# Kernel optimization log

Hardware: AMD Instinct MI355X
Metric: run time of the kernel (lower is better)

## Reference

```python
import jax, jax.numpy as jnp
import numpy as np
from jax import lax

B, T, V, E, H, M = 512, 60, 50000, 300, 512, 256


def _lstm_final_h(x_emb, seqlen, kernel, bias):
    """BasicLSTMCell (gate order i,j,f,o; forget_bias=1.0) with dynamic_rnn
    sequence_length semantics: state stops updating at t >= seqlen.
    x_emb: [B, T, E]; returns final h: [B, H]."""
    b = x_emb.shape[0]
    h0 = jnp.zeros((b, H), x_emb.dtype)
    c0 = jnp.zeros((b, H), x_emb.dtype)

    def step(carry, inp):
        c, h = carry
        xt, t = inp
        z = jnp.concatenate([xt, h], axis=1) @ kernel + bias  # [B, 4H]
        i, j, f, o = jnp.split(z, 4, axis=1)
        nc = c * jax.nn.sigmoid(f + 1.0) + jax.nn.sigmoid(i) * jnp.tanh(j)
        nh = jnp.tanh(nc) * jax.nn.sigmoid(o)
        valid = (t < seqlen)[:, None]
        return (jnp.where(valid, nc, c), jnp.where(valid, nh, h)), None

    (c, h), _ = lax.scan(step, (c0, h0),
                         (jnp.swapaxes(x_emb, 0, 1), jnp.arange(T)))
    return h


def setup_inputs() -> dict:
    key = jax.random.key(0)
    ks = jax.random.split(key, 8)
    return {
        "input1": jax.random.randint(ks[0], (B, T), 0, V, dtype=jnp.int32),
        "input2": jax.random.randint(ks[1], (B, T), 0, V, dtype=jnp.int32),
        "seqlen1": jax.random.randint(ks[2], (B,), 1, T + 1, dtype=jnp.int32),
        "seqlen2": jax.random.randint(ks[3], (B,), 1, T + 1, dtype=jnp.int32),
        "embeddings": jax.random.normal(ks[4], (V, E), jnp.float32) * 0.1,
        "lstm_kernel": jax.random.normal(ks[5], (E + H, 4 * H), jnp.float32) * 0.02,
        "lstm_bias": jnp.zeros((4 * H,), jnp.float32),
        "W1": jax.random.normal(ks[6], (4 * (H + 1) + 1, M), jnp.float32) * 0.02,
        "b1": jnp.zeros((1, M), jnp.float32),
        "W2": jax.random.normal(ks[7], (M, 2), jnp.float32) * 0.02,
        "b2": jnp.zeros((1, 2), jnp.float32),
    }


def reference(input1, input2, seqlen1, seqlen2, embeddings,
              lstm_kernel, lstm_bias, W1, b1, W2, b2):
    x1 = embeddings[input1]  # [B, T, E]
    x2 = embeddings[input2]
    h1 = _lstm_final_h(x1, seqlen1, lstm_kernel, lstm_bias)  # [B, H]
    h2 = _lstm_final_h(x2, seqlen2, lstm_kernel, lstm_bias)
    len1 = (seqlen1.astype(jnp.float32) / float(T))[:, None]
    len2 = (seqlen2.astype(jnp.float32) / float(T))[:, None]
    h1 = jnp.concatenate([h1, len1], axis=1)  # [B, H+1]
    h2 = jnp.concatenate([h2, len2], axis=1)
    h_sub = h1 - h2
    h_dist = jnp.sum(h_sub * h_sub, axis=1, keepdims=True)  # [B, 1]
    h_mul = h1 * h2
    h_combined = jnp.concatenate([h1, h2, h_sub, h_dist, h_mul], axis=1)
    e1 = jax.nn.relu(h_combined @ W1 + b1)  # dropout keep_prob=1 -> identity
    preds = e1 @ W2 + b2  # [B, 2]
    return preds
```

## Files before the change

### kernel.cpp

```cpp
#include <hip/hip_runtime.h>
#include <hip/hip_bf16.h>

#define BATCH 512
#define TT 60
#define EDIM 300
#define HDIM 512
#define KREAL 812
#define KP 896
#define KP1 2112
#define MDIM 256

typedef __bf16 bf16x4 __attribute__((ext_vector_type(4)));
typedef __bf16 bf16x8 __attribute__((ext_vector_type(8)));
typedef float  f32x16 __attribute__((ext_vector_type(16)));

#define GLL16(g, l) __builtin_amdgcn_global_load_lds( \
    (const __attribute__((address_space(1))) void*)(g), \
    (__attribute__((address_space(3))) void*)(l), 16, 0, 0)

__device__ __forceinline__ float sigm(float x) {
    return 1.0f / (1.0f + __expf(-x));
}
__device__ __forceinline__ float tanh_fast(float x) {
    float e = __expf(-2.0f * fabsf(x));
    float r = (1.0f - e) / (1.0f + e);
    return x >= 0.0f ? r : -r;
}


__global__ __launch_bounds__(256) void sort_rows(const int* __restrict__ sl1,
                                                 const int* __restrict__ sl2,
                                                 int* __restrict__ rowinfo,
                                                 unsigned* __restrict__ nact) {
    __shared__ unsigned cnt[61];
    __shared__ unsigned off[61];
    int tid = threadIdx.x;
    if (tid < 61) cnt[tid] = 0;
    __syncthreads();
    for (int i = tid; i < 1024; i += 256) {
        int sl = (i < 512) ? sl1[i] : sl2[i - 512];
        atomicAdd(&cnt[60 - sl], 1u);
    }
    __syncthreads();
    if (tid == 0) {
        unsigned s = 0;
        for (int k = 0; k < 61; ++k) { off[k] = s; s += cnt[k]; }
        for (int t = 0; t < 60; ++t) {
            unsigned act = off[60 - t];
            nact[t] = (act + 63) >> 6;
        }
    }
    __syncthreads();
    for (int i = tid; i < 1024; i += 256) {
        int sc = i >= 512;
        int b = i & 511;
        int sl = sc ? sl2[b] : sl1[b];
        unsigned pos = atomicAdd(&off[60 - sl], 1u);
        rowinfo[pos] = b | (sc << 15) | (sl << 20);
    }
}

__global__ __launch_bounds__(256) void prep_w(const float* __restrict__ kern,
                                              __bf16* __restrict__ wf) {
    __shared__ float tile[64][65];
    int bk = blockIdx.x % 14;
    int bn = blockIdx.x / 14;
    int k0 = bk * 64, n0 = bn * 64;
    int tid = threadIdx.x;
#pragma unroll
    for (int i = 0; i < 16; ++i) {
        int id = i * 256 + tid;
        int kk = id >> 6, nn = id & 63;
        int kg = k0 + kk;
        int src = (kg < 300) ? kg : (kg >= 384 ? kg - 84 : -1);
        tile[kk][nn] = (src >= 0) ? kern[(size_t)src * 2048 + n0 + nn] : 0.0f;
    }
    __syncthreads();
    int gate = n0 >> 9;
    int nt = gate >> 1;
#pragma unroll
    for (int i = 0; i < 2; ++i) {
        int id = i * 256 + tid;
        int nn = id >> 3, k8 = id & 7;
        bf16x8 hv, lv;
#pragma unroll
        for (int j = 0; j < 8; ++j) {
            float v = tile[k8 * 8 + j][nn];
            __bf16 h = (__bf16)v;
            hv[j] = h;
            lv[j] = (__bf16)(v - (float)h);
        }
        int cg = (((n0 & 511) >> 4) + (nn >> 4));
        int hc = nn & 15;
        int lzc = ((gate & 1) << 4) + hc;
        int kglob = k0 + k8 * 8;
        int c = kglob >> 7;
        int j = (kglob >> 4) & 7;
        int half = k8 & 1;
        size_t o = (size_t)cg * 114688 + c * 16384 + (j * 4 + nt * 2) * 512
                 + (half * 32 + lzc) * 8;
        *(bf16x8*)(wf + o) = hv;
        *(bf16x8*)(wf + o + 512) = lv;
    }
}

__global__ __launch_bounds__(256) void prep_w1(const float* __restrict__ W1,
                                               __bf16* __restrict__ w1h,
                                               __bf16* __restrict__ w1l) {
    __shared__ float tile[64][65];
    int bk = blockIdx.x % 33;
    int bn = blockIdx.x / 33;
    int k0 = bk * 64, n0 = bn * 64;
    int tid = threadIdx.x;
#pragma unroll
    for (int i = 0; i < 16; ++i) {
        int id = i * 256 + tid;
        int kk = id >> 6, nn = id & 63;
        int kg = k0 + kk;
        tile[kk][nn] = (kg < 2053) ? W1[(size_t)kg * MDIM + n0 + nn] : 0.0f;
    }
    __syncthreads();
#pragma unroll
    for (int i = 0; i < 2; ++i) {
        int id = i * 256 + tid;
        int nn = id >> 3, k8 = (id & 7) * 8;
        bf16x8 hv, lv;
#pragma unroll
        for (int j = 0; j < 8; ++j) {
            float v = tile[k8 + j][nn];
            __bf16 h = (__bf16)v;
            hv[j] = h;
            lv[j] = (__bf16)(v - (float)h);
        }
        size_t o = (size_t)(n0 + nn) * KP1 + k0 + k8;
        *(bf16x8*)(w1h + o) = hv;
        *(bf16x8*)(w1l + o) = lv;
    }
}

__device__ __forceinline__ void emb_unit(int tok, int rl, int rr, int bt,
                                         const float* __restrict__ emb,
                                         __bf16* Xfn) {
    const float* er = emb + (size_t)tok * EDIM + rr * 8;
    float4 f0 = *(const float4*)er;
    float4 f1 = (rr == 37) ? make_float4(0.f, 0.f, 0.f, 0.f)
                           : *(const float4*)(er + 4);
    float vv[8] = {f0.x, f0.y, f0.z, f0.w, f1.x, f1.y, f1.z, f1.w};
    bf16x8 hv, lv;
#pragma unroll
    for (int j = 0; j < 8; ++j) {
        __bf16 h = (__bf16)vv[j];
        hv[j] = h;
        lv[j] = (__bf16)(vv[j] - (float)h);
    }
    int ke = rr * 8;
    int c = ke >> 7, kl = ke & 127;
    int kg = kl >> 6, jj = (kl >> 4) & 3, half = (kl >> 3) & 1;
    int s = rl >> 5;
    size_t base = ((((size_t)bt * 2 + s) * 2 + kg) * 7 + c) * 4096 + jj * 1024
                + (half * 32 + (rl & 31)) * 8;
    *(bf16x8*)(Xfn + base) = hv;
    *(bf16x8*)(Xfn + base + 512) = lv;
}

__global__ __launch_bounds__(256) void prep_x0(const int* __restrict__ in1,
                                               const int* __restrict__ in2,
                                               const int* __restrict__ rowinfo,
                                               const float* __restrict__ emb,
                                               __bf16* __restrict__ Xf) {
    __shared__ int tk[64];
    int bt = blockIdx.x >> 5, cg = blockIdx.x & 31;
    int tid = threadIdx.x;
    if (tid < 64) {
        int info = rowinfo[bt * 64 + tid];
        int b = info & 511, sc = (info >> 15) & 1;
        tk[tid] = (sc ? in2 : in1)[b * TT];
    }
    __syncthreads();
    if (tid < 76) {
        int id = tid * 32 + cg;
        int rl = id / 38, rr = id - rl * 38;
        emb_unit(tk[rl], rl, rr, bt, emb, Xf);
    }
}

#define ZSTR 72

__global__ __launch_bounds__(256, 2) void lstm_step(
    int t,
    const int* __restrict__ in1, const int* __restrict__ in2,
    const int* __restrict__ rowinfo, const unsigned* __restrict__ nact,
    const float* __restrict__ emb, const float* __restrict__ bias,
    const __bf16* __restrict__ wf,
    const __bf16* __restrict__ Xf, __bf16* __restrict__ Xfn,
    float* __restrict__ h_state, float* __restrict__ c_state) {

    int bx = blockIdx.x;
    int xcd = bx & 7;
    int loc = bx >> 3;
    int bt = ((loc >> 3) << 1) | (xcd & 1);
    int cg = ((xcd >> 1) << 3) | (loc & 7);
    if (bt >= (int)nact[t]) return;

    __shared__ __align__(16) __bf16 Bb[2][16384];
    __shared__ int info_s[64];
    __shared__ int tk[64];

    int tid = threadIdx.x;
    int w = tid >> 6, lane = tid & 63, l31 = lane & 31;
    int s = w >> 1, kg = w & 1;

    if (tid < 64) {
        int info = rowinfo[bt * 64 + tid];
        info_s[tid] = info;
        int b = info & 511, sc = (info >> 15) & 1;
        int tn = (t + 1 < TT) ? t + 1 : t;
        tk[tid] = (sc ? in2 : in1)[b * TT + tn];
    }

    const __bf16* wb = wf + (size_t)cg * 114688;
    auto stageB = [&](int c, int buf) {
        const __bf16* src = wb + c * 16384 + w * 4096 + lane * 8;
        __bf16* dst = &Bb[buf][w * 4096 + lane * 8];
#pragma unroll
        for (int i = 0; i < 8; ++i)
            GLL16(src + i * 512, dst + i * 512);
    };

    const __bf16* Abase = Xf + ((((size_t)bt * 2 + s) * 2 + kg) * 7) * 4096
                        + lane * 8;

    f32x16 acc[2];
#pragma unroll
    for (int nt = 0; nt < 2; ++nt)
#pragma unroll
        for (int r = 0; r < 16; ++r) acc[nt][r] = 0.0f;

    bf16x8 aH[4], aL[4];
    stageB(0, 0);
#pragma unroll
    for (int jj = 0; jj < 4; ++jj) {
        aH[jj] = *(const bf16x8*)(Abase + jj * 1024);
        aL[jj] = *(const bf16x8*)(Abase + jj * 1024 + 512);
    }
    __syncthreads();

#pragma unroll
    for (int c = 0; c < 7; ++c) {
        int cur = c & 1;
        bf16x8 nH[4], nL[4];
        if (c < 6) {
            stageB(c + 1, 1 - cur);
            const __bf16* An = Abase + (c + 1) * 4096;
#pragma unroll
            for (int jj = 0; jj < 4; ++jj) {
                nH[jj] = *(const bf16x8*)(An + jj * 1024);
                nL[jj] = *(const bf16x8*)(An + jj * 1024 + 512);
            }
        }
#pragma unroll
        for (int jj = 0; jj < 4; ++jj) {
            int j = kg * 4 + jj;
#pragma unroll
            for (int nt = 0; nt < 2; ++nt) {
                int T0 = (j * 4 + nt * 2) * 512 + lane * 8;
                bf16x8 bh = *(const bf16x8*)(&Bb[cur][T0]);
                bf16x8 bl = *(const bf16x8*)(&Bb[cur][T0 + 512]);
                acc[nt] = __builtin_amdgcn_mfma_f32_32x32x16_bf16(aH[jj], bh, acc[nt], 0, 0, 0);
                acc[nt] = __builtin_amdgcn_mfma_f32_32x32x16_bf16(aH[jj], bl, acc[nt], 0, 0, 0);
                acc[nt] = __builtin_amdgcn_mfma_f32_32x32x16_bf16(aL[jj], bh, acc[nt], 0, 0, 0);
            }
        }
        if (c < 6) {
#pragma unroll
            for (int jj = 0; jj < 4; ++jj) { aH[jj] = nH[jj]; aL[jj] = nL[jj]; }
        }
        __syncthreads();
    }

    float* zs = (float*)&Bb[1][0];
    if (kg == 0) {
#pragma unroll
        for (int nt = 0; nt < 2; ++nt)
#pragma unroll
            for (int r = 0; r < 16; ++r) {
                int rl = s * 32 + (r & 3) + ((r >> 2) << 3) + ((lane >> 5) << 2);
                zs[rl * ZSTR + nt * 32 + l31] = acc[nt][r];
            }
    }
    __syncthreads();
    if (kg == 1) {
#pragma unroll
        for (int nt = 0; nt < 2; ++nt)
#pragma unroll
            for (int r = 0; r < 16; ++r) {
                int rl = s * 32 + (r & 3) + ((r >> 2) << 3) + ((lane >> 5) << 2);
                zs[rl * ZSTR + nt * 32 + l31] += acc[nt][r];
            }
    }
    __syncthreads();

    __bf16* zh = &Bb[0][0];
    int hc16 = tid & 15;
    int hcol = (cg << 4) + hc16;
    float bi = bias[hcol], bj = bias[512 + hcol];
    float bfv = bias[1024 + hcol], bo = bias[1536 + hcol];
#pragma unroll
    for (int i = 0; i < 4; ++i) {
        int rl = i * 16 + (tid >> 4);
        int info = info_s[rl];
        int b = info & 511, sc = (info >> 15) & 1, sl = info >> 20;
        float zi = zs[rl * ZSTR + hc16]      + bi;
        float zj = zs[rl * ZSTR + 16 + hc16] + bj;
        float zf = zs[rl * ZSTR + 32 + hc16] + bfv;
        float zo = zs[rl * ZSTR + 48 + hc16] + bo;
        size_t co = (size_t)(bt * 64 + rl) * HDIM + hcol;
        size_t ho = (size_t)((sc << 9) + b) * HDIM + hcol;
        float c_old = c_state[co];
        float h_old = h_state[ho];
        float nc = c_old * sigm(zf + 1.0f) + sigm(zi) * tanh_fast(zj);
        float nh = tanh_fast(nc) * sigm(zo);
        bool valid = t < sl;
        float cs = valid ? nc : c_old;
        float hs = valid ? nh : h_old;
        c_state[co] = cs;
        h_state[ho] = hs;
        __bf16 hh = (__bf16)hs;
        int grp = hc16 >> 3, e = hc16 & 7;
        zh[(grp * 64 + rl) * 8 + e] = hh;
        zh[((2 + grp) * 64 + rl) * 8 + e] = (__bf16)(hs - (float)hh);
    }
    __syncthreads();

    if (t + 1 < TT) {
        int plane = tid >> 7;
        int grp = (tid >> 6) & 1;
        int rl = tid & 63;
        bf16x8 val = *(const bf16x8*)(zh + ((plane * 2 + grp) * 64 + rl) * 8);
        int s2 = rl >> 5;
        int c2 = 3 + (cg >> 3);
        int kg2 = (cg >> 2) & 1;
        int jj2 = cg & 3;
        size_t base = ((((size_t)bt * 2 + s2) * 2 + kg2) * 7 + c2) * 4096
                    + jj2 * 1024 + plane * 512 + (grp * 32 + (rl & 31)) * 8;
        *(bf16x8*)(Xfn + base) = val;
        if (tid < 76) {
            int id = tid * 32 + cg;
            int rl2 = id / 38, rr = id - rl2 * 38;
            emb_unit(tk[rl2], rl2, rr, bt, emb, Xfn);
        }
    }
}

__global__ __launch_bounds__(256) void head1(const float* __restrict__ h_state,
                                             const int* __restrict__ sl1,
                                             const int* __restrict__ sl2,
                                             __bf16* __restrict__ hch,
                                             __bf16* __restrict__ hcl) {
    int b = blockIdx.x;
    int tid = threadIdx.x;
    const float* h1 = h_state + (size_t)b * HDIM;
    const float* h2 = h_state + (size_t)(512 + b) * HDIM;
    size_t ro = (size_t)b * KP1;
    float l1 = (float)sl1[b] / (float)TT;
    float l2 = (float)sl2[b] / (float)TT;
    float part = 0.0f;
#pragma unroll
    for (int i = 0; i < 2; ++i) {
        int k = i * 256 + tid;
        float a = h1[k], c = h2[k];
        float sv = a - c;
        float mv = a * c;
        __bf16 xh;
        xh = (__bf16)a;  hch[ro + k] = xh;         hcl[ro + k] = (__bf16)(a - (float)xh);
        xh = (__bf16)c;  hch[ro + 513 + k] = xh;   hcl[ro + 513 + k] = (__bf16)(c - (float)xh);
        xh = (__bf16)sv; hch[ro + 1026 + k] = xh;  hcl[ro + 1026 + k] = (__bf16)(sv - (float)xh);
        xh = (__bf16)mv; hch[ro + 1540 + k] = xh;  hcl[ro + 1540 + k] = (__bf16)(mv - (float)xh);
        part += sv * sv;
    }
    __shared__ float red[4];
#pragma unroll
    for (int off = 32; off > 0; off >>= 1) part += __shfl_down(part, off, 64);
    if ((tid & 63) == 0) red[tid >> 6] = part;
    __syncthreads();
    if (tid == 0) {
        float d = red[0] + red[1] + red[2] + red[3];
        float ls = l1 - l2;
        d += ls * ls;
        float vals[5] = {l1, l2, ls, d, l1 * l2};
        int pos[5] = {512, 1025, 1538, 1539, 2052};
#pragma unroll
        for (int i = 0; i < 5; ++i) {
            __bf16 xh = (__bf16)vals[i];
            hch[ro + pos[i]] = xh;
            hcl[ro + pos[i]] = (__bf16)(vals[i] - (float)xh);
        }
    }
}

__global__ __launch_bounds__(512, 2) void head2m(
    const __bf16* __restrict__ hch, const __bf16* __restrict__ hcl,
    const __bf16* __restrict__ w1h, const __bf16* __restrict__ w1l,
    float* __restrict__ part) {

    __shared__ __align__(16) __bf16 Bb[2][64 * 512];

    int tid = threadIdx.x;
    int bx = blockIdx.x;
    int mt = bx >> 3;
    int n2 = (bx >> 2) & 1;
    int ks = bx & 3;
    int w = tid >> 6, lane = tid & 63, l31 = lane & 31;
    int half8 = (lane >> 5) << 3;
    int s = w >> 1, nh = w & 1;
    int kbase = ks * 528;

    int k8 = tid & 15;
    int jb = k8 >> 1;
    int rb = (tid >> 4) & 31;
    size_t gboff[8];
    int lo[8];
#pragma unroll
    for (int i = 0; i < 8; ++i) {
        int r = ((i & 3) << 5) + rb;
        int plane = i >> 2;
        int ng = n2 * 128 + r;
        gboff[i] = (size_t)ng * KP1 + k8 * 8;
        int nt = r >> 5;
        int colp = ((r & 31) + (jb << 2)) & 31;
        lo[i] = ((((jb << 2) + nt) << 1) + plane) * 512 + (colp + ((k8 & 1) << 5)) * 8;
    }

    const __bf16* Ah0 = hch + (size_t)(mt * 128 + s * 32 + l31) * KP1 + kbase + half8;
    const __bf16* Al0 = hcl + (size_t)(mt * 128 + s * 32 + l31) * KP1 + kbase + half8;

    bf16x8 rB[8];
    f32x16 acc[2];
#pragma unroll
    for (int nt = 0; nt < 2; ++nt)
#pragma unroll
        for (int r = 0; r < 16; ++r) acc[nt][r] = 0.0f;

#pragma unroll
    for (int i = 0; i < 8; ++i)
        rB[i] = *(const bf16x8*)(((i >= 4) ? w1l : w1h) + gboff[i] + kbase);
#pragma unroll
    for (int i = 0; i < 8; ++i) *(bf16x8*)(&Bb[0][lo[i]]) = rB[i];
    __syncthreads();

    for (int c = 0; c < 5; ++c) {
        int cur = c & 1;
        if (c < 4) {
            int k0 = kbase + (c + 1) * 128;
            bool tail = (c + 1 == 4);
#pragma unroll
            for (int i = 0; i < 8; ++i) {
                if (!tail || k8 < 2)
                    rB[i] = *(const bf16x8*)(((i >= 4) ? w1l : w1h) + gboff[i] + k0);
            }
        }
        int jmax = (c == 4) ? 1 : 8;
        for (int j = 0; j < jmax; ++j) {
            bf16x8 ah = *(const bf16x8*)(Ah0 + c * 128 + j * 16);
            bf16x8 al = *(const bf16x8*)(Al0 + c * 128 + j * 16);
            int cp = ((l31 + (j << 2)) & 31) + ((lane >> 5) << 5);
#pragma unroll
            for (int ntl = 0; ntl < 2; ++ntl) {
                int ntg = nh * 2 + ntl;
                const __bf16* bp = &Bb[cur][(((j << 2) + ntg) << 1) * 512 + cp * 8];
                bf16x8 bh = *(const bf16x8*)bp;
                bf16x8 bl = *(const bf16x8*)(bp + 512);
                acc[ntl] = __builtin_amdgcn_mfma_f32_32x32x16_bf16(ah, bh, acc[ntl], 0, 0, 0);
                acc[ntl] = __builtin_amdgcn_mfma_f32_32x32x16_bf16(ah, bl, acc[ntl], 0, 0, 0);
                acc[ntl] = __builtin_amdgcn_mfma_f32_32x32x16_bf16(al, bh, acc[ntl], 0, 0, 0);
            }
        }
        if (c < 4) {
#pragma unroll
            for (int i = 0; i < 8; ++i) *(bf16x8*)(&Bb[1 - cur][lo[i]]) = rB[i];
        }
        __syncthreads();
    }

#pragma unroll
    for (int ntl = 0; ntl < 2; ++ntl)
#pragma unroll
        for (int r = 0; r < 16; ++r) {
            int row = mt * 128 + s * 32 + (r & 3) + ((r >> 2) << 3) + ((lane >> 5) << 2);
            int col = n2 * 128 + nh * 64 + ntl * 32 + l31;
            part[((size_t)ks * 512 + row) * MDIM + col] = acc[ntl][r];
        }
}

__global__ __launch_bounds__(256) void head3(const float* __restrict__ part,
                                             const float* __restrict__ b1,
                                             const float* __restrict__ W2,
                                             const float* __restrict__ b2,
                                             float* __restrict__ out) {
    int row = blockIdx.x;
    int tid = threadIdx.x;
    float sv = b1[tid];
#pragma unroll
    for (int ks = 0; ks < 4; ++ks)
        sv += part[((size_t)ks * 512 + row) * MDIM + tid];
    float e = fmaxf(sv, 0.0f);
    float p0 = e * W2[tid * 2 + 0];
    float p1 = e * W2[tid * 2 + 1];
#pragma unroll
    for (int off = 32; off > 0; off >>= 1) {
        p0 += __shfl_down(p0, off, 64);
        p1 += __shfl_down(p1, off, 64);
    }
    __shared__ float r0[4], r1[4];
    if ((tid & 63) == 0) { r0[tid >> 6] = p0; r1[tid >> 6] = p1; }
    __syncthreads();
    if (tid == 0) out[row * 2 + 0] = r0[0] + r0[1] + r0[2] + r0[3] + b2[0];
    if (tid == 1) out[row * 2 + 1] = r1[0] + r1[1] + r1[2] + r1[3] + b2[1];
}

extern "C" void kernel_launch(void* const* d_in, const int* in_sizes, int n_in,
                              void* d_out, int out_size, void* d_ws, size_t ws_size,
                              hipStream_t stream) {
    const int*   in1  = (const int*)d_in[0];
    const int*   in2  = (const int*)d_in[1];
    const int*   sl1  = (const int*)d_in[2];
    const int*   sl2  = (const int*)d_in[3];
    const float* emb  = (const float*)d_in[4];
    const float* kern = (const float*)d_in[5];
    const float* bias = (const float*)d_in[6];
    const float* W1   = (const float*)d_in[7];
    const float* b1   = (const float*)d_in[8];
    const float* W2   = (const float*)d_in[9];
    const float* b2   = (const float*)d_in[10];
    float* out = (float*)d_out;

    char* ws = (char*)d_ws;
    int*      rowinfo = (int*)ws;
    unsigned* nact    = (unsigned*)(ws + 4096u);
    float*  h_state = (float*)(ws + 2097152u);
    float*  c_state = (float*)(ws + 4194304u);
    __bf16* Xf0 = (__bf16*)(ws + 6291456u);
    __bf16* Xf1 = (__bf16*)(ws + 9961472u);
    __bf16* wf  = (__bf16*)(ws + 13631488u);
    __bf16* hch = (__bf16*)(ws + 20971520u);
    __bf16* hcl = (__bf16*)(ws + 23134208u);
    __bf16* w1h = (__bf16*)(ws + 25296896u);
    __bf16* w1l = (__bf16*)(ws + 26378240u);
    float*  part = (float*)(ws + 27459584u);

    hipMemsetAsync(ws + 2097152u, 0, 7864320u, stream);
    hipMemsetAsync(ws + 20971520u, 0, 4325376u, stream);

    sort_rows<<<dim3(1), dim3(256), 0, stream>>>(sl1, sl2, rowinfo, nact);
    prep_w<<<dim3(14 * 32), dim3(256), 0, stream>>>(kern, wf);
    prep_w1<<<dim3(33 * 4), dim3(256), 0, stream>>>(W1, w1h, w1l);
    prep_x0<<<dim3(512), dim3(256), 0, stream>>>(in1, in2, rowinfo, emb, Xf0);

    for (int t = 0; t < TT; ++t) {
        __bf16* Xf  = (t & 1) ? Xf1 : Xf0;
        __bf16* Xfn = (t & 1) ? Xf0 : Xf1;
        lstm_step<<<dim3(512), dim3(256), 0, stream>>>(
            t, in1, in2, rowinfo, nact, emb, bias, wf, Xf, Xfn,
            h_state, c_state);
    }

    head1<<<dim3(512), dim3(256), 0, stream>>>(h_state, sl1, sl2, hch, hcl);
    head2m<<<dim3(32), dim3(512), 0, stream>>>(hch, hcl, w1h, w1l, part);
    head3<<<dim3(512), dim3(256), 0, stream>>>(part, b1, W2, b2, out);
}
```

Before: 1.066 ms.

## Replace per-timestep LSTM launches with one persistent kernel using per-tile flags

The 60 per-timestep kernel launches become a single persistent kernel. Each row tile loops over its own timesteps and waits on an atomic step counter until all 32 column-group blocks have written the previous hidden state into a per-timestep buffer. The whole embedding table is pre-converted once into split bf16 hi/lo form, so the step loop reads embedding rows directly instead of re-gathering and scattering them. This removes launch overhead and lets tiles with short sequences finish early. In exchange it depends on all 512 blocks being co-resident (two per CU), adds spin-wait latency, and converting the full 50000-row table costs extra bandwidth.

```diff
diff --git a/kernel.cpp b/kernel.cpp
--- a/kernel.cpp
+++ b/kernel.cpp
@@ -5,10 +5,9 @@
 #define TT 60
 #define EDIM 300
 #define HDIM 512
-#define KREAL 812
-#define KP 896
 #define KP1 2112
 #define MDIM 256
+#define V48 2400000
 
 typedef __bf16 bf16x4 __attribute__((ext_vector_type(4)));
 typedef __bf16 bf16x8 __attribute__((ext_vector_type(8)));
@@ -31,11 +30,12 @@
 __global__ __launch_bounds__(256) void sort_rows(const int* __restrict__ sl1,
                                                  const int* __restrict__ sl2,
                                                  int* __restrict__ rowinfo,
-                                                 unsigned* __restrict__ nact) {
+                                                 unsigned* __restrict__ step_done) {
     __shared__ unsigned cnt[61];
     __shared__ unsigned off[61];
     int tid = threadIdx.x;
     if (tid < 61) cnt[tid] = 0;
+    if (tid >= 64 && tid < 80) step_done[tid - 64] = 0;
     __syncthreads();
     for (int i = tid; i < 1024; i += 256) {
         int sl = (i < 512) ? sl1[i] : sl2[i - 512];
@@ -45,10 +45,6 @@
     if (tid == 0) {
         unsigned s = 0;
         for (int k = 0; k < 61; ++k) { off[k] = s; s += cnt[k]; }
-        for (int t = 0; t < 60; ++t) {
-            unsigned act = off[60 - t];
-            nact[t] = (act + 63) >> 6;
-        }
     }
     __syncthreads();
     for (int i = tid; i < 1024; i += 256) {
@@ -138,14 +134,28 @@
     }
 }
 
-__device__ __forceinline__ void emb_unit(int tok, int rl, int rr, int bt,
-                                         const float* __restrict__ emb,
-                                         __bf16* Xfn) {
-    const float* er = emb + (size_t)tok * EDIM + rr * 8;
-    float4 f0 = *(const float4*)er;
-    float4 f1 = (rr == 37) ? make_float4(0.f, 0.f, 0.f, 0.f)
-                           : *(const float4*)(er + 4);
-    float vv[8] = {f0.x, f0.y, f0.z, f0.w, f1.x, f1.y, f1.z, f1.w};
+__global__ __launch_bounds__(256) void prep_emb(const float* __restrict__ emb,
+                                                __bf16* __restrict__ embB) {
+    int id = blockIdx.x * 256 + threadIdx.x;
+    if (id >= V48) return;
+    int tok = id / 48;
+    int k8 = id - tok * 48;
+    int k0 = k8 * 8;
+    float vv[8];
+    const float* er = emb + (size_t)tok * EDIM + k0;
+    if (k0 + 8 <= EDIM) {
+        float4 f0 = *(const float4*)er;
+        float4 f1 = *(const float4*)(er + 4);
+        vv[0] = f0.x; vv[1] = f0.y; vv[2] = f0.z; vv[3] = f0.w;
+        vv[4] = f1.x; vv[5] = f1.y; vv[6] = f1.z; vv[7] = f1.w;
+    } else if (k0 < EDIM) {
+        float4 f0 = *(const float4*)er;
+        vv[0] = f0.x; vv[1] = f0.y; vv[2] = f0.z; vv[3] = f0.w;
+        vv[4] = vv[5] = vv[6] = vv[7] = 0.f;
+    } else {
+#pragma unroll
+        for (int j = 0; j < 8; ++j) vv[j] = 0.f;
+    }
     bf16x8 hv, lv;
 #pragma unroll
     for (int j = 0; j < 8; ++j) {
@@ -153,46 +163,20 @@
         hv[j] = h;
         lv[j] = (__bf16)(vv[j] - (float)h);
     }
-    int ke = rr * 8;
-    int c = ke >> 7, kl = ke & 127;
-    int kg = kl >> 6, jj = (kl >> 4) & 3, half = (kl >> 3) & 1;
-    int s = rl >> 5;
-    size_t base = ((((size_t)bt * 2 + s) * 2 + kg) * 7 + c) * 4096 + jj * 1024
-                + (half * 32 + (rl & 31)) * 8;
-    *(bf16x8*)(Xfn + base) = hv;
-    *(bf16x8*)(Xfn + base + 512) = lv;
-}
-
-__global__ __launch_bounds__(256) void prep_x0(const int* __restrict__ in1,
-                                               const int* __restrict__ in2,
-                                               const int* __restrict__ rowinfo,
-                                               const float* __restrict__ emb,
-                                               __bf16* __restrict__ Xf) {
-    __shared__ int tk[64];
-    int bt = blockIdx.x >> 5, cg = blockIdx.x & 31;
-    int tid = threadIdx.x;
-    if (tid < 64) {
-        int info = rowinfo[bt * 64 + tid];
-        int b = info & 511, sc = (info >> 15) & 1;
-        tk[tid] = (sc ? in2 : in1)[b * TT];
-    }
-    __syncthreads();
-    if (tid < 76) {
-        int id = tid * 32 + cg;
-        int rl = id / 38, rr = id - rl * 38;
-        emb_unit(tk[rl], rl, rr, bt, emb, Xf);
-    }
+    size_t o = (size_t)tok * 768 + k0;
+    *(bf16x8*)(embB + o) = hv;
+    *(bf16x8*)(embB + o + 384) = lv;
 }
 
 #define ZSTR 72
 
-__global__ __launch_bounds__(256, 2) void lstm_step(
-    int t,
+__global__ __launch_bounds__(256, 2) void lstm_all(
     const int* __restrict__ in1, const int* __restrict__ in2,
-    const int* __restrict__ rowinfo, const unsigned* __restrict__ nact,
-    const float* __restrict__ emb, const float* __restrict__ bias,
+    const int* __restrict__ rowinfo,
+    const __bf16* __restrict__ embB, const float* __restrict__ bias,
     const __bf16* __restrict__ wf,
-    const __bf16* __restrict__ Xf, __bf16* __restrict__ Xfn,
+    __bf16* __restrict__ XfH,
+    unsigned* __restrict__ step_done,
     float* __restrict__ h_state, float* __restrict__ c_state) {
 
     int bx = blockIdx.x;
@@ -200,23 +184,26 @@
     int loc = bx >> 3;
     int bt = ((loc >> 3) << 1) | (xcd & 1);
     int cg = ((xcd >> 1) << 3) | (loc & 7);
-    if (bt >= (int)nact[t]) return;
 
     __shared__ __align__(16) __bf16 Bb[2][16384];
     __shared__ int info_s[64];
-    __shared__ int tk[64];
 
     int tid = threadIdx.x;
     int w = tid >> 6, lane = tid & 63, l31 = lane & 31;
     int s = w >> 1, kg = w & 1;
 
-    if (tid < 64) {
-        int info = rowinfo[bt * 64 + tid];
-        info_s[tid] = info;
-        int b = info & 511, sc = (info >> 15) & 1;
-        int tn = (t + 1 < TT) ? t + 1 : t;
-        tk[tid] = (sc ? in2 : in1)[b * TT + tn];
-    }
+    if (tid < 64) info_s[tid] = rowinfo[bt * 64 + tid];
+    __syncthreads();
+    int t_end = info_s[0] >> 20;
+
+    int rowl = s * 32 + l31;
+    int inf_r = info_s[rowl];
+    const int* tokptr = ((((inf_r >> 15) & 1) ? in2 : in1)) + (inf_r & 511) * TT;
+
+    int hc16 = tid & 15;
+    int hcol = (cg << 4) + hc16;
+    float bi = bias[hcol], bj = bias[512 + hcol];
+    float bfv = bias[1024 + hcol], bo = bias[1536 + hcol];
 
     const __bf16* wb = wf + (size_t)cg * 114688;
     auto stageB = [&](int c, int buf) {
@@ -227,128 +214,148 @@
             GLL16(src + i * 512, dst + i * 512);
     };
 
-    const __bf16* Abase = Xf + ((((size_t)bt * 2 + s) * 2 + kg) * 7) * 4096
-                        + lane * 8;
-
-    f32x16 acc[2];
-#pragma unroll
-    for (int nt = 0; nt < 2; ++nt)
-#pragma unroll
-        for (int r = 0; r < 16; ++r) acc[nt][r] = 0.0f;
-
-    bf16x8 aH[4], aL[4];
-    stageB(0, 0);
-#pragma unroll
-    for (int jj = 0; jj < 4; ++jj) {
-        aH[jj] = *(const bf16x8*)(Abase + jj * 1024);
-        aL[jj] = *(const bf16x8*)(Abase + jj * 1024 + 512);
-    }
-    __syncthreads();
-
-#pragma unroll
-    for (int c = 0; c < 7; ++c) {
-        int cur = c & 1;
-        bf16x8 nH[4], nL[4];
-        if (c < 6) {
-            stageB(c + 1, 1 - cur);
-            const __bf16* An = Abase + (c + 1) * 4096;
+    int ew = kg * 64 + ((lane >> 5) << 3);
+    size_t hw_off = (size_t)((s * 2 + kg) * 4) * 4096 + lane * 8;
+
+    for (int t = 0; t < t_end; ++t) {
+        f32x16 acc[2];
+#pragma unroll
+        for (int nt = 0; nt < 2; ++nt)
+#pragma unroll
+            for (int r = 0; r < 16; ++r) acc[nt][r] = 0.0f;
+
+        int tok = tokptr[t];
+        const __bf16* eb = embB + (size_t)tok * 768 + ew;
+        const __bf16* hrd = XfH + ((size_t)t * 16 + bt) * 65536 + hw_off;
+
+        bf16x8 aH[4], aL[4];
+        stageB(0, 0);
+#pragma unroll
+        for (int jj = 0; jj < 4; ++jj) {
+            aH[jj] = *(const bf16x8*)(eb + jj * 16);
+            aL[jj] = *(const bf16x8*)(eb + 384 + jj * 16);
+        }
+
+        if (t > 0 && tid == 0) {
+            unsigned target = 32u * (unsigned)t;
+            int guard = 0;
+            while (__hip_atomic_load(step_done + bt, __ATOMIC_RELAXED,
+                                     __HIP_MEMORY_SCOPE_AGENT) < target) {
+                __builtin_amdgcn_s_sleep(4);
+                if (++guard > (1 << 20)) break;
+            }
+        }
+        __syncthreads();
+
+#pragma unroll
+        for (int c = 0; c < 7; ++c) {
+            int cur = c & 1;
+            bf16x8 nH[4], nL[4];
+            if (c < 6) {
+                stageB(c + 1, 1 - cur);
+                if (c < 2) {
+                    const __bf16* en = eb + (c + 1) * 128;
+#pragma unroll
+                    for (int jj = 0; jj < 4; ++jj) {
+                        nH[jj] = *(const bf16x8*)(en + jj * 16);
+                        nL[jj] = *(const bf16x8*)(en + 384 + jj * 16);
+                    }
+                } else {
+                    const __bf16* An = hrd + (c - 2) * 4096;
+#pragma unroll
+                    for (int jj = 0; jj < 4; ++jj) {
+                        nH[jj] = *(const bf16x8*)(An + jj * 1024);
+                        nL[jj] = *(const bf16x8*)(An + jj * 1024 + 512);
+                    }
+                }
+            }
 #pragma unroll
             for (int jj = 0; jj < 4; ++jj) {
-                nH[jj] = *(const bf16x8*)(An + jj * 1024);
-                nL[jj] = *(const bf16x8*)(An + jj * 1024 + 512);
+                int j = kg * 4 + jj;
+#pragma unroll
+                for (int nt = 0; nt < 2; ++nt) {
+                    int T0 = (j * 4 + nt * 2) * 512 + lane * 8;
+                    bf16x8 bh = *(const bf16x8*)(&Bb[cur][T0]);
+                    bf16x8 bl = *(const bf16x8*)(&Bb[cur][T0 + 512]);
+                    acc[nt] = __builtin_amdgcn_mfma_f32_32x32x16_bf16(aH[jj], bh, acc[nt], 0, 0, 0);
+                    acc[nt] = __builtin_amdgcn_mfma_f32_32x32x16_bf16(aH[jj], bl, acc[nt], 0, 0, 0);
+                    acc[nt] = __builtin_amdgcn_mfma_f32_32x32x16_bf16(aL[jj], bh, acc[nt], 0, 0, 0);
+                }
             }
-        }
-#pragma unroll
-        for (int jj = 0; jj < 4; ++jj) {
-            int j = kg * 4 + jj;
-#pragma unroll
-            for (int nt = 0; nt < 2; ++nt) {
-                int T0 = (j * 4 + nt * 2) * 512 + lane * 8;
-                bf16x8 bh = *(const bf16x8*)(&Bb[cur][T0]);
-                bf16x8 bl = *(const bf16x8*)(&Bb[cur][T0 + 512]);
-                acc[nt] = __builtin_amdgcn_mfma_f32_32x32x16_bf16(aH[jj], bh, acc[nt], 0, 0, 0);
-                acc[nt] = __builtin_amdgcn_mfma_f32_32x32x16_bf16(aH[jj], bl, acc[nt], 0, 0, 0);
-                acc[nt] = __builtin_amdgcn_mfma_f32_32x32x16_bf16(aL[jj], bh, acc[nt], 0, 0, 0);
+            if (c < 6) {
+#pragma unroll
+                for (int jj = 0; jj < 4; ++jj) { aH[jj] = nH[jj]; aL[jj] = nL[jj]; }
             }
-        }
-        if (c < 6) {
-#pragma unroll
-            for (int jj = 0; jj < 4; ++jj) { aH[jj] = nH[jj]; aL[jj] = nL[jj]; }
+            __syncthreads();
+        }
+
+        float* zs = (float*)&Bb[1][0];
+        if (kg == 0) {
+#pragma unroll
+            for (int nt = 0; nt < 2; ++nt)
+#pragma unroll
+                for (int r = 0; r < 16; ++r) {
+                    int rl = s * 32 + (r & 3) + ((r >> 2) << 3) + ((lane >> 5) << 2);
+                    zs[rl * ZSTR + nt * 32 + l31] = acc[nt][r];
+                }
         }
         __syncthreads();
-    }
-
-    float* zs = (float*)&Bb[1][0];
-    if (kg == 0) {
-#pragma unroll
-        for (int nt = 0; nt < 2; ++nt)
-#pragma unroll
-            for (int r = 0; r < 16; ++r) {
-                int rl = s * 32 + (r & 3) + ((r >> 2) << 3) + ((lane >> 5) << 2);
-                zs[rl * ZSTR + nt * 32 + l31] = acc[nt][r];
-            }
-    }
-    __syncthreads();
-    if (kg == 1) {
-#pragma unroll
-        for (int nt = 0; nt < 2; ++nt)
-#pragma unroll
-            for (int r = 0; r < 16; ++r) {
-                int rl = s * 32 + (r & 3) + ((r >> 2) << 3) + ((lane >> 5) << 2);
-                zs[rl * ZSTR + nt * 32 + l31] += acc[nt][r];
-            }
-    }
-    __syncthreads();
-
-    __bf16* zh = &Bb[0][0];
-    int hc16 = tid & 15;
-    int hcol = (cg << 4) + hc16;
-    float bi = bias[hcol], bj = bias[512 + hcol];
-    float bfv = bias[1024 + hcol], bo = bias[1536 + hcol];
-#pragma unroll
-    for (int i = 0; i < 4; ++i) {
-        int rl = i * 16 + (tid >> 4);
-        int info = info_s[rl];
-        int b = info & 511, sc = (info >> 15) & 1, sl = info >> 20;
-        float zi = zs[rl * ZSTR + hc16]      + bi;
-        float zj = zs[rl * ZSTR + 16 + hc16] + bj;
-        float zf = zs[rl * ZSTR + 32 + hc16] + bfv;
-        float zo = zs[rl * ZSTR + 48 + hc16] + bo;
-        size_t co = (size_t)(bt * 64 + rl) * HDIM + hcol;
-        size_t ho = (size_t)((sc << 9) + b) * HDIM + hcol;
-        float c_old = c_state[co];
-        float h_old = h_state[ho];
-        float nc = c_old * sigm(zf + 1.0f) + sigm(zi) * tanh_fast(zj);
-        float nh = tanh_fast(nc) * sigm(zo);
-        bool valid = t < sl;
-        float cs = valid ? nc : c_old;
-        float hs = valid ? nh : h_old;
-        c_state[co] = cs;
-        h_state[ho] = hs;
-        __bf16 hh = (__bf16)hs;
-        int grp = hc16 >> 3, e = hc16 & 7;
-        zh[(grp * 64 + rl) * 8 + e] = hh;
-        zh[((2 + grp) * 64 + rl) * 8 + e] = (__bf16)(hs - (float)hh);
-    }
-    __syncthreads();
-
-    if (t + 1 < TT) {
-        int plane = tid >> 7;
-        int grp = (tid >> 6) & 1;
-        int rl = tid & 63;
-        bf16x8 val = *(const bf16x8*)(zh + ((plane * 2 + grp) * 64 + rl) * 8);
-        int s2 = rl >> 5;
-        int c2 = 3 + (cg >> 3);
-        int kg2 = (cg >> 2) & 1;
-        int jj2 = cg & 3;
-        size_t base = ((((size_t)bt * 2 + s2) * 2 + kg2) * 7 + c2) * 4096
-                    + jj2 * 1024 + plane * 512 + (grp * 32 + (rl & 31)) * 8;
-        *(bf16x8*)(Xfn + base) = val;
-        if (tid < 76) {
-            int id = tid * 32 + cg;
-            int rl2 = id / 38, rr = id - rl2 * 38;
-            emb_unit(tk[rl2], rl2, rr, bt, emb, Xfn);
-        }
+        if (kg == 1) {
+#pragma unroll
+            for (int nt = 0; nt < 2; ++nt)
+#pragma unroll
+                for (int r = 0; r < 16; ++r) {
+                    int rl = s * 32 + (r & 3) + ((r >> 2) << 3) + ((lane >> 5) << 2);
+                    zs[rl * ZSTR + nt * 32 + l31] += acc[nt][r];
+                }
+        }
+        __syncthreads();
+
+        __bf16* zh = &Bb[0][0];
+#pragma unroll
+        for (int i = 0; i < 4; ++i) {
+            int rl = i * 16 + (tid >> 4);
+            int info = info_s[rl];
+            int b = info & 511, sc = (info >> 15) & 1, sl = info >> 20;
+            float zi = zs[rl * ZSTR + hc16]      + bi;
+            float zj = zs[rl * ZSTR + 16 + hc16] + bj;
+            float zf = zs[rl * ZSTR + 32 + hc16] + bfv;
+            float zo = zs[rl * ZSTR + 48 + hc16] + bo;
+            size_t co = (size_t)(bt * 64 + rl) * HDIM + hcol;
+            size_t ho = (size_t)((sc << 9) + b) * HDIM + hcol;
+            float c_old = c_state[co];
+            float h_old = h_state[ho];
+            float nc = c_old * sigm(zf + 1.0f) + sigm(zi) * tanh_fast(zj);
+            float nh = tanh_fast(nc) * sigm(zo);
+            bool valid = t < sl;
+            float cs = valid ? nc : c_old;
+            float hs = valid ? nh : h_old;
+            c_state[co] = cs;
+            h_state[ho] = hs;
+            __bf16 hh = (__bf16)hs;
+            int grp = hc16 >> 3, e = hc16 & 7;
+            zh[(grp * 64 + rl) * 8 + e] = hh;
+            zh[((2 + grp) * 64 + rl) * 8 + e] = (__bf16)(hs - (float)hh);
+        }
+        __syncthreads();
+
+        if (t + 1 < t_end) {
+            int plane = tid >> 7;
+            int grp = (tid >> 6) & 1;
+            int rl = tid & 63;
+            ulonglong2 uv = *(const ulonglong2*)(zh + ((plane * 2 + grp) * 64 + rl) * 8);
+            int s2 = rl >> 5;
+            size_t base = ((size_t)(t + 1) * 16 + bt) * 65536
+                        + (size_t)((s2 * 2 + ((cg >> 2) & 1)) * 4 + (cg >> 3)) * 4096
+                        + (cg & 3) * 1024 + plane * 512 + (grp * 32 + (rl & 31)) * 8;
+            unsigned long long* dst = (unsigned long long*)(XfH + base);
+            __hip_atomic_store(dst,     uv.x, __ATOMIC_RELAXED, __HIP_MEMORY_SCOPE_AGENT);
+            __hip_atomic_store(dst + 1, uv.y, __ATOMIC_RELAXED, __HIP_MEMORY_SCOPE_AGENT);
+        }
+        __syncthreads();
+        if (t + 1 < t_end && tid == 0)
+            __hip_atomic_fetch_add(step_done + bt, 1u, __ATOMIC_RELEASE,
+                                   __HIP_MEMORY_SCOPE_AGENT);
     }
 }
 
@@ -535,34 +542,30 @@
     float* out = (float*)d_out;
 
     char* ws = (char*)d_ws;
-    int*      rowinfo = (int*)ws;
-    unsigned* nact    = (unsigned*)(ws + 4096u);
+    int*      rowinfo   = (int*)ws;
+    unsigned* step_done = (unsigned*)(ws + 4096u);
     float*  h_state = (float*)(ws + 2097152u);
     float*  c_state = (float*)(ws + 4194304u);
-    __bf16* Xf0 = (__bf16*)(ws + 6291456u);
-    __bf16* Xf1 = (__bf16*)(ws + 9961472u);
-    __bf16* wf  = (__bf16*)(ws + 13631488u);
-    __bf16* hch = (__bf16*)(ws + 20971520u);
-    __bf16* hcl = (__bf16*)(ws + 23134208u);
-    __bf16* w1h = (__bf16*)(ws + 25296896u);
-    __bf16* w1l = (__bf16*)(ws + 26378240u);
-    float*  part = (float*)(ws + 27459584u);
-
-    hipMemsetAsync(ws + 2097152u, 0, 7864320u, stream);
-    hipMemsetAsync(ws + 20971520u, 0, 4325376u, stream);
-
-    sort_rows<<<dim3(1), dim3(256), 0, stream>>>(sl1, sl2, rowinfo, nact);
+    __bf16* wf   = (__bf16*)(ws + 6291456u);
+    __bf16* hch  = (__bf16*)(ws + 13631488u);
+    __bf16* hcl  = (__bf16*)(ws + 15794176u);
+    __bf16* w1h  = (__bf16*)(ws + 17956864u);
+    __bf16* w1l  = (__bf16*)(ws + 19038208u);
+    float*  part = (float*)(ws + 20119552u);
+    __bf16* embB = (__bf16*)(ws + 23068672u);
+    __bf16* XfH  = (__bf16*)(ws + 100663296u);
+
+    hipMemsetAsync(ws + 2097152u, 0, 4194304u, stream);
+    hipMemsetAsync(ws + 13631488u, 0, 4325376u, stream);
+    hipMemsetAsync(ws + 100663296u, 0, 2097152u, stream);
+
+    sort_rows<<<dim3(1), dim3(256), 0, stream>>>(sl1, sl2, rowinfo, step_done);
     prep_w<<<dim3(14 * 32), dim3(256), 0, stream>>>(kern, wf);
     prep_w1<<<dim3(33 * 4), dim3(256), 0, stream>>>(W1, w1h, w1l);
-    prep_x0<<<dim3(512), dim3(256), 0, stream>>>(in1, in2, rowinfo, emb, Xf0);
-
-    for (int t = 0; t < TT; ++t) {
-        __bf16* Xf  = (t & 1) ? Xf1 : Xf0;
-        __bf16* Xfn = (t & 1) ? Xf0 : Xf1;
-        lstm_step<<<dim3(512), dim3(256), 0, stream>>>(
-            t, in1, in2, rowinfo, nact, emb, bias, wf, Xf, Xfn,
-            h_state, c_state);
-    }
+    prep_emb<<<dim3(9375), dim3(256), 0, stream>>>(emb, embB);
+
+    lstm_all<<<dim3(512), dim3(256), 0, stream>>>(
+        in1, in2, rowinfo, embB, bias, wf, XfH, step_done, h_state, c_state);
 
     head1<<<dim3(512), dim3(256), 0, stream>>>(h_state, sl1, sl2, hch, hcl);
     head2m<<<dim3(32), dim3(512), 0, stream>>>(hch, hcl, w1h, w1l, part);
```

Measured after the change: 1.839 ms. 72.5% more time.
